# Performance work log

Hardware: AMD Instinct MI355X
Metric: run time of the kernel (lower is better)

## Reference

```python
import jax, jax.numpy as jnp
import numpy as np

N_NODES = 50000
N_EDGES = 640000
DIM_IN = 128
DIM_OUT = 128
NUM_GRAPHS = 64


def setup_inputs() -> dict:
    key = jax.random.key(0)
    ks = jax.random.split(key, 8)
    x = jax.random.normal(ks[0], (N_NODES, DIM_IN), dtype=jnp.float32)
    edge_index = jax.random.randint(ks[1], (2, N_EDGES), 0, N_NODES, dtype=jnp.int32)
    batch = jnp.sort(jax.random.randint(ks[2], (N_NODES,), 0, NUM_GRAPHS, dtype=jnp.int32))
    s = 1.0 / np.sqrt(DIM_IN)
    W1 = jax.random.normal(ks[3], (DIM_IN, DIM_IN), dtype=jnp.float32) * s
    W2 = jax.random.normal(ks[4], (DIM_IN, DIM_IN), dtype=jnp.float32) * s
    Wlin = jax.random.normal(ks[5], (DIM_IN, DIM_OUT), dtype=jnp.float32) * s
    b1 = jnp.zeros((DIM_IN,), jnp.float32)
    b2 = jnp.zeros((DIM_IN,), jnp.float32)
    blin = jnp.zeros((DIM_OUT,), jnp.float32)
    return {"x": x, "edge_index": edge_index, "batch": batch,
            "W1": W1, "b1": b1, "W2": W2, "b2": b2, "Wlin": Wlin, "blin": blin}


def _gcn_conv(x, W, b, src, dst, n_nodes):
    # GCNConv: symmetric norm with self-loops: D^{-1/2}(A+I)D^{-1/2} X W + b
    h = x @ W                                                   # [N, d]
    deg = jax.ops.segment_sum(jnp.ones_like(dst, jnp.float32), dst,
                              num_segments=n_nodes) + 1.0       # +1 self loop
    dinv = jax.lax.rsqrt(deg)                                   # [N]
    w = dinv[src] * dinv[dst]                                   # per-edge norm [E]
    agg = jax.ops.segment_sum(h[src] * w[:, None], dst, num_segments=n_nodes)
    return agg + h * (dinv * dinv)[:, None] + b                 # self-loop term + bias


def reference(x, edge_index, batch, W1, b1, W2, b2, Wlin, blin):
    n = x.shape[0]
    src, dst = edge_index[0], edge_index[1]
    h = jax.nn.relu(_gcn_conv(x, W1, b1, src, dst, n))          # dropout = identity (eval)
    h = _gcn_conv(h, W2, b2, src, dst, n)
    # global mean pool over graphs
    s = jax.ops.segment_sum(h, batch, num_segments=NUM_GRAPHS)  # [G, d]
    cnt = jax.ops.segment_sum(jnp.ones((n,), jnp.float32), batch, num_segments=NUM_GRAPHS)
    pooled = s / jnp.maximum(cnt, 1.0)[:, None]
    return jax.nn.relu(pooled @ Wlin + blin)
```

## Files before the change

### kernel.cpp

```cpp
#include <hip/hip_runtime.h>

#define N_NODES   50000
#define N_EDGES   640000
#define DIM       128
#define NUM_GRAPHS 64
#define SLOTS     64

typedef __attribute__((ext_vector_type(8))) short          s16x8;
typedef __attribute__((ext_vector_type(8))) unsigned short u16x8;
typedef __attribute__((ext_vector_type(4))) float          f32x4;

__device__ inline float bf2f(unsigned short u) {
    unsigned v = ((unsigned)u) << 16;
    float f;
    __builtin_memcpy(&f, &v, 4);
    return f;
}
__device__ inline unsigned short f2bf(float f) {
    unsigned u;
    __builtin_memcpy(&u, &f, 4);
    u = (u + 0x7fffu + ((u >> 16) & 1u)) >> 16;
    return (unsigned short)u;
}

__global__ __launch_bounds__(128) void k_prep_w(const float* __restrict__ W1,
                                                const float* __restrict__ W2,
                                                unsigned short* __restrict__ Wt1,
                                                unsigned short* __restrict__ Wt2,
                                                int* __restrict__ cnt,
                                                float* __restrict__ pooled) {
    int k = blockIdx.x & 127;
    const float*    W  = (blockIdx.x < DIM) ? W1 : W2;
    unsigned short* Wt = (blockIdx.x < DIM) ? Wt1 : Wt2;
    int n = threadIdx.x;
    Wt[n * DIM + k] = f2bf(W[k * DIM + n]);

    int gid = blockIdx.x * 128 + threadIdx.x;
    for (int i = gid; i < N_NODES; i += 32768) cnt[i] = 0;
    if (gid < NUM_GRAPHS * DIM) pooled[gid] = 0.f;
}

__global__ __launch_bounds__(256) void k_fill_slots(const int* __restrict__ src,
                                                    const int* __restrict__ dst,
                                                    int* __restrict__ cnt,
                                                    unsigned short* __restrict__ slots) {
    int e0 = (blockIdx.x * blockDim.x + threadIdx.x) * 4;
    if (e0 >= N_EDGES) return;
    int4 s4 = *reinterpret_cast<const int4*>(src + e0);
    int4 d4 = *reinterpret_cast<const int4*>(dst + e0);
    int p0 = atomicAdd(&cnt[d4.x], 1);
    int p1 = atomicAdd(&cnt[d4.y], 1);
    int p2 = atomicAdd(&cnt[d4.z], 1);
    int p3 = atomicAdd(&cnt[d4.w], 1);
    if (p0 < SLOTS) slots[d4.x * SLOTS + p0] = (unsigned short)s4.x;
    if (p1 < SLOTS) slots[d4.y * SLOTS + p1] = (unsigned short)s4.y;
    if (p2 < SLOTS) slots[d4.z * SLOTS + p2] = (unsigned short)s4.z;
    if (p3 < SLOTS) slots[d4.w * SLOTS + p3] = (unsigned short)s4.w;
}

template<int A_F32>
__global__ __launch_bounds__(512) void k_gemm_mfma(const void* __restrict__ Ain,
                                                   const unsigned short* __restrict__ Wt,
                                                   unsigned short* __restrict__ H,
                                                   int M) {
    __shared__ unsigned short wsh[DIM][136];
    const int tid = threadIdx.x;

    #pragma unroll
    for (int i = 0; i < 4; i++) {
        int off = tid * 8 + i * 4096;
        int r = off >> 7, cc = off & 127;
        u16x8 v = *reinterpret_cast<const u16x8*>(Wt + off);
        *reinterpret_cast<u16x8*>(&wsh[r][cc]) = v;
    }
    __syncthreads();

    const int wid  = tid >> 6;
    const int lane = tid & 63;
    const int l15  = lane & 15;
    const int lk   = lane >> 4;
    const int row0 = blockIdx.x * 256 + wid * 32;

    f32x4 acc[2][8];
    #pragma unroll
    for (int a = 0; a < 2; a++)
        #pragma unroll
        for (int n = 0; n < 8; n++) acc[a][n] = (f32x4){0.f, 0.f, 0.f, 0.f};

    const long long r0 = min(row0 + l15,      M - 1);
    const long long r1 = min(row0 + 16 + l15, M - 1);

    #pragma unroll
    for (int kk = 0; kk < 4; kk++) {
        const int kb = kk * 32 + lk * 8;
        s16x8 a0, a1;
        if (A_F32) {
            const float* Af = (const float*)Ain;
            const float4 p0 = *reinterpret_cast<const float4*>(Af + r0 * DIM + kb);
            const float4 q0 = *reinterpret_cast<const float4*>(Af + r0 * DIM + kb + 4);
            const float4 p1 = *reinterpret_cast<const float4*>(Af + r1 * DIM + kb);
            const float4 q1 = *reinterpret_cast<const float4*>(Af + r1 * DIM + kb + 4);
            a0[0]=(short)f2bf(p0.x); a0[1]=(short)f2bf(p0.y); a0[2]=(short)f2bf(p0.z); a0[3]=(short)f2bf(p0.w);
            a0[4]=(short)f2bf(q0.x); a0[5]=(short)f2bf(q0.y); a0[6]=(short)f2bf(q0.z); a0[7]=(short)f2bf(q0.w);
            a1[0]=(short)f2bf(p1.x); a1[1]=(short)f2bf(p1.y); a1[2]=(short)f2bf(p1.z); a1[3]=(short)f2bf(p1.w);
            a1[4]=(short)f2bf(q1.x); a1[5]=(short)f2bf(q1.y); a1[6]=(short)f2bf(q1.z); a1[7]=(short)f2bf(q1.w);
        } else {
            const unsigned short* Ab = (const unsigned short*)Ain;
            a0 = *reinterpret_cast<const s16x8*>(Ab + r0 * DIM + kb);
            a1 = *reinterpret_cast<const s16x8*>(Ab + r1 * DIM + kb);
        }
        #pragma unroll
        for (int n = 0; n < 8; n++) {
            s16x8 b = *reinterpret_cast<const s16x8*>(&wsh[n * 16 + l15][kb]);
            acc[0][n] = __builtin_amdgcn_mfma_f32_16x16x32_bf16(a0, b, acc[0][n], 0, 0, 0);
            acc[1][n] = __builtin_amdgcn_mfma_f32_16x16x32_bf16(a1, b, acc[1][n], 0, 0, 0);
        }
    }

    #pragma unroll
    for (int rh = 0; rh < 2; rh++) {
        #pragma unroll
        for (int j = 0; j < 4; j++) {
            int row = row0 + rh * 16 + lk * 4 + j;
            if (row < M) {
                #pragma unroll
                for (int n = 0; n < 8; n++)
                    H[(long long)row * DIM + n * 16 + l15] = f2bf(acc[rh][n][j]);
            }
        }
    }
}

__device__ inline void gather_node(const int* __restrict__ cnt,
                                   const unsigned short* __restrict__ slots,
                                   const unsigned short* __restrict__ h,
                                   const float* __restrict__ bias,
                                   int n, int c, float dn, float* acc) {
    float d2 = dn * dn;
    u16x8 hv = *reinterpret_cast<const u16x8*>(h + (size_t)n * DIM + c);
    #pragma unroll
    for (int j = 0; j < 8; j++) acc[j] = bf2f(hv[j]) * d2 + bias[c + j];

    const int m = min(cnt[n], SLOTS);
    const unsigned short* sl = slots + (size_t)n * SLOTS;

    int i = 0;
    for (; i + 3 < m; i += 4) {
        int s0 = sl[i], s1 = sl[i + 1], s2 = sl[i + 2], s3 = sl[i + 3];
        float w0 = rsqrtf((float)cnt[s0] + 1.0f) * dn;
        float w1 = rsqrtf((float)cnt[s1] + 1.0f) * dn;
        float w2 = rsqrtf((float)cnt[s2] + 1.0f) * dn;
        float w3 = rsqrtf((float)cnt[s3] + 1.0f) * dn;
        u16x8 v0 = *reinterpret_cast<const u16x8*>(h + (size_t)s0 * DIM + c);
        u16x8 v1 = *reinterpret_cast<const u16x8*>(h + (size_t)s1 * DIM + c);
        u16x8 v2 = *reinterpret_cast<const u16x8*>(h + (size_t)s2 * DIM + c);
        u16x8 v3 = *reinterpret_cast<const u16x8*>(h + (size_t)s3 * DIM + c);
        #pragma unroll
        for (int j = 0; j < 8; j++)
            acc[j] += (bf2f(v0[j]) * w0 + bf2f(v1[j]) * w1) +
                      (bf2f(v2[j]) * w2 + bf2f(v3[j]) * w3);
    }
    for (; i < m; i++) {
        int s0 = sl[i];
        float w0 = rsqrtf((float)cnt[s0] + 1.0f) * dn;
        u16x8 v0 = *reinterpret_cast<const u16x8*>(h + (size_t)s0 * DIM + c);
        #pragma unroll
        for (int j = 0; j < 8; j++) acc[j] += bf2f(v0[j]) * w0;
    }
}

__global__ __launch_bounds__(256) void k_pull1(const int* __restrict__ cnt,
                                               const unsigned short* __restrict__ slots,
                                               const unsigned short* __restrict__ h,
                                               const float* __restrict__ bias,
                                               unsigned short* __restrict__ outp) {
    int gid = blockIdx.x * blockDim.x + threadIdx.x;
    int n = gid >> 4;
    if (n >= N_NODES) return;
    int c = (gid & 15) << 3;

    float dn = rsqrtf((float)cnt[n] + 1.0f);
    float acc[8];
    gather_node(cnt, slots, h, bias, n, c, dn, acc);

    u16x8 o;
    #pragma unroll
    for (int j = 0; j < 8; j++) o[j] = f2bf(fmaxf(acc[j], 0.f));
    *reinterpret_cast<u16x8*>(outp + (size_t)n * DIM + c) = o;
}

__global__ __launch_bounds__(256) void k_pull_pool(const int* __restrict__ cnt,
                                                   const unsigned short* __restrict__ slots,
                                                   const unsigned short* __restrict__ h,
                                                   const float* __restrict__ bias,
                                                   const int* __restrict__ batch,
                                                   float* __restrict__ pooled) {
    __shared__ float pool_l[2][DIM];
    const int tid  = threadIdx.x;
    const int base = blockIdx.x * 16;
    const int n    = base + (tid >> 4);
    const int c    = (tid & 15) << 3;

    pool_l[tid >> 7][tid & 127] = 0.f;
    __syncthreads();

    float dn = rsqrtf((float)cnt[n] + 1.0f);
    float acc[8];
    gather_node(cnt, slots, h, bias, n, c, dn, acc);

    const int g    = batch[n];
    const int gmin = batch[base];
    const int d    = g - gmin;

    if (__all(g == __shfl(g, 0))) {
        #pragma unroll
        for (int j = 0; j < 8; j++) {
            acc[j] += __shfl_xor(acc[j], 16);
            acc[j] += __shfl_xor(acc[j], 32);
        }
        if ((tid & 63) < 16) {
            if (d < 2) {
                #pragma unroll
                for (int j = 0; j < 8; j++) atomicAdd(&pool_l[d][c + j], acc[j]);
            } else {
                #pragma unroll
                for (int j = 0; j < 8; j++) atomicAdd(&pooled[g * DIM + c + j], acc[j]);
            }
        }
    } else {
        if (d < 2) {
            #pragma unroll
            for (int j = 0; j < 8; j++) atomicAdd(&pool_l[d][c + j], acc[j]);
        } else {
            #pragma unroll
            for (int j = 0; j < 8; j++) atomicAdd(&pooled[g * DIM + c + j], acc[j]);
        }
    }
    __syncthreads();

    const int f = tid & 127;
    if (tid < 128) {
        atomicAdd(&pooled[gmin * DIM + f], pool_l[0][f]);
    } else {
        int gmax = batch[base + 15];
        if (gmax > gmin) atomicAdd(&pooled[(gmin + 1) * DIM + f], pool_l[1][f]);
    }
}

__global__ __launch_bounds__(128) void k_pool2(const float* __restrict__ pooled,
                                               const int* __restrict__ batch,
                                               const float* __restrict__ Wlin,
                                               const float* __restrict__ blin,
                                               float* __restrict__ out) {
    int g = blockIdx.x;
    int t = threadIdx.x;
    __shared__ int se[2];
    __shared__ float pr[DIM];
    if (t < 2) {
        int target = g + t;
        int lo = 0, hi = N_NODES;
        while (lo < hi) { int mid = (lo + hi) >> 1; if (batch[mid] < target) lo = mid + 1; else hi = mid; }
        se[t] = lo;
    }
    __syncthreads();
    float inv_cnt = 1.0f / fmaxf((float)(se[1] - se[0]), 1.0f);
    pr[t] = pooled[g * DIM + t] * inv_cnt;
    __syncthreads();
    float acc = blin[t];
    #pragma unroll 8
    for (int k = 0; k < DIM; k++) acc += pr[k] * Wlin[k * DIM + t];
    out[g * DIM + t] = fmaxf(acc, 0.f);
}

extern "C" void kernel_launch(void* const* d_in, const int* in_sizes, int n_in,
                              void* d_out, int out_size, void* d_ws, size_t ws_size,
                              hipStream_t stream) {
    const float* x          = (const float*)d_in[0];
    const int*   edge_index = (const int*)d_in[1];
    const int*   batch      = (const int*)d_in[2];
    const float* W1         = (const float*)d_in[3];
    const float* b1         = (const float*)d_in[4];
    const float* W2         = (const float*)d_in[5];
    const float* b2         = (const float*)d_in[6];
    const float* Wlin       = (const float*)d_in[7];
    const float* blin       = (const float*)d_in[8];
    float*       out        = (float*)d_out;

    const int* src = edge_index;
    const int* dst = edge_index + N_EDGES;

    char* ws = (char*)d_ws;
    size_t off = 0;
    auto alloc = [&](size_t bytes) { void* p = ws + off; off = (off + bytes + 255) & ~255ULL; return p; };
    int*            cnt    = (int*)            alloc((size_t)N_NODES * 4);
    unsigned short* slots  = (unsigned short*) alloc((size_t)N_NODES * SLOTS * 2);
    float*          pooled = (float*)          alloc((size_t)NUM_GRAPHS * DIM * 4);
    unsigned short* Wt1    = (unsigned short*) alloc((size_t)DIM * DIM * 2);
    unsigned short* Wt2    = (unsigned short*) alloc((size_t)DIM * DIM * 2);
    unsigned short* H1     = (unsigned short*) alloc((size_t)N_NODES * DIM * 2);
    unsigned short* Z1     = (unsigned short*) alloc((size_t)N_NODES * DIM * 2);
    unsigned short* H2     = (unsigned short*) alloc((size_t)N_NODES * DIM * 2);

    const int fillBlocks = (N_EDGES / 4 + 255) / 256;
    const int pullBlocks = (N_NODES * 16 + 255) / 256;
    const int gemmBlocks = (N_NODES + 255) / 256;

    k_prep_w<<<2 * DIM, DIM, 0, stream>>>(W1, W2, Wt1, Wt2, cnt, pooled);

    k_fill_slots<<<fillBlocks, 256, 0, stream>>>(src, dst, cnt, slots);

    k_gemm_mfma<1><<<gemmBlocks, 512, 0, stream>>>(x, Wt1, H1, N_NODES);
    k_pull1<<<pullBlocks, 256, 0, stream>>>(cnt, slots, H1, b1, Z1);

    k_gemm_mfma<0><<<gemmBlocks, 512, 0, stream>>>(Z1, Wt2, H2, N_NODES);
    k_pull_pool<<<pullBlocks, 256, 0, stream>>>(cnt, slots, H2, b2, batch, pooled);

    k_pool2<<<NUM_GRAPHS, 128, 0, stream>>>(pooled, batch, Wlin, blin, out);
}
```

Measured before the change: 127.4 us.

## Fuse edge-slot fill with first GEMM and layer-1 gather with second GEMM

The edge-slot fill and the first node GEMM now run as one launch, with a block-index split: the first blocks do the GEMM and the rest do the atomic slot fill. The layer-1 aggregation is fused with the second GEMM. Each block gathers 32 nodes into LDS and multiplies them by W2 with MFMA, so the Z1 intermediate is never written to or read from global memory. This removes two launches and a full N×128 bf16 round trip through memory. In exchange, the second GEMM reads W2 from global memory per wave rather than from LDS, and it uses small 32-row tiles.

```diff
diff --git a/kernel.cpp b/kernel.cpp
--- a/kernel.cpp
+++ b/kernel.cpp
@@ -5,6 +5,8 @@
 #define DIM       128
 #define NUM_GRAPHS 64
 #define SLOTS     64
+#define GEMM1_BLOCKS 196
+#define FILL_BLOCKS  313
 
 typedef __attribute__((ext_vector_type(8))) short          s16x8;
 typedef __attribute__((ext_vector_type(8))) unsigned short u16x8;
@@ -40,37 +42,37 @@
     if (gid < NUM_GRAPHS * DIM) pooled[gid] = 0.f;
 }
 
-__global__ __launch_bounds__(256) void k_fill_slots(const int* __restrict__ src,
+__global__ __launch_bounds__(512) void k_fill_gemm1(const int* __restrict__ src,
                                                     const int* __restrict__ dst,
                                                     int* __restrict__ cnt,
-                                                    unsigned short* __restrict__ slots) {
-    int e0 = (blockIdx.x * blockDim.x + threadIdx.x) * 4;
-    if (e0 >= N_EDGES) return;
-    int4 s4 = *reinterpret_cast<const int4*>(src + e0);
-    int4 d4 = *reinterpret_cast<const int4*>(dst + e0);
-    int p0 = atomicAdd(&cnt[d4.x], 1);
-    int p1 = atomicAdd(&cnt[d4.y], 1);
-    int p2 = atomicAdd(&cnt[d4.z], 1);
-    int p3 = atomicAdd(&cnt[d4.w], 1);
-    if (p0 < SLOTS) slots[d4.x * SLOTS + p0] = (unsigned short)s4.x;
-    if (p1 < SLOTS) slots[d4.y * SLOTS + p1] = (unsigned short)s4.y;
-    if (p2 < SLOTS) slots[d4.z * SLOTS + p2] = (unsigned short)s4.z;
-    if (p3 < SLOTS) slots[d4.w * SLOTS + p3] = (unsigned short)s4.w;
-}
-
-template<int A_F32>
-__global__ __launch_bounds__(512) void k_gemm_mfma(const void* __restrict__ Ain,
-                                                   const unsigned short* __restrict__ Wt,
-                                                   unsigned short* __restrict__ H,
-                                                   int M) {
+                                                    unsigned short* __restrict__ slots,
+                                                    const float* __restrict__ x,
+                                                    const unsigned short* __restrict__ Wt1,
+                                                    unsigned short* __restrict__ H1) {
     __shared__ unsigned short wsh[DIM][136];
     const int tid = threadIdx.x;
+
+    if (blockIdx.x >= GEMM1_BLOCKS) {
+        int e0 = ((blockIdx.x - GEMM1_BLOCKS) * 512 + tid) * 4;
+        if (e0 >= N_EDGES) return;
+        int4 s4 = *reinterpret_cast<const int4*>(src + e0);
+        int4 d4 = *reinterpret_cast<const int4*>(dst + e0);
+        int p0 = atomicAdd(&cnt[d4.x], 1);
+        int p1 = atomicAdd(&cnt[d4.y], 1);
+        int p2 = atomicAdd(&cnt[d4.z], 1);
+        int p3 = atomicAdd(&cnt[d4.w], 1);
+        if (p0 < SLOTS) slots[d4.x * SLOTS + p0] = (unsigned short)s4.x;
+        if (p1 < SLOTS) slots[d4.y * SLOTS + p1] = (unsigned short)s4.y;
+        if (p2 < SLOTS) slots[d4.z * SLOTS + p2] = (unsigned short)s4.z;
+        if (p3 < SLOTS) slots[d4.w * SLOTS + p3] = (unsigned short)s4.w;
+        return;
+    }
 
     #pragma unroll
     for (int i = 0; i < 4; i++) {
         int off = tid * 8 + i * 4096;
         int r = off >> 7, cc = off & 127;
-        u16x8 v = *reinterpret_cast<const u16x8*>(Wt + off);
+        u16x8 v = *reinterpret_cast<const u16x8*>(Wt1 + off);
         *reinterpret_cast<u16x8*>(&wsh[r][cc]) = v;
     }
     __syncthreads();
@@ -87,28 +89,21 @@
         #pragma unroll
         for (int n = 0; n < 8; n++) acc[a][n] = (f32x4){0.f, 0.f, 0.f, 0.f};
 
-    const long long r0 = min(row0 + l15,      M - 1);
-    const long long r1 = min(row0 + 16 + l15, M - 1);
+    const long long r0 = min(row0 + l15,      N_NODES - 1);
+    const long long r1 = min(row0 + 16 + l15, N_NODES - 1);
 
     #pragma unroll
     for (int kk = 0; kk < 4; kk++) {
         const int kb = kk * 32 + lk * 8;
         s16x8 a0, a1;
-        if (A_F32) {
-            const float* Af = (const float*)Ain;
-            const float4 p0 = *reinterpret_cast<const float4*>(Af + r0 * DIM + kb);
-            const float4 q0 = *reinterpret_cast<const float4*>(Af + r0 * DIM + kb + 4);
-            const float4 p1 = *reinterpret_cast<const float4*>(Af + r1 * DIM + kb);
-            const float4 q1 = *reinterpret_cast<const float4*>(Af + r1 * DIM + kb + 4);
-            a0[0]=(short)f2bf(p0.x); a0[1]=(short)f2bf(p0.y); a0[2]=(short)f2bf(p0.z); a0[3]=(short)f2bf(p0.w);
-            a0[4]=(short)f2bf(q0.x); a0[5]=(short)f2bf(q0.y); a0[6]=(short)f2bf(q0.z); a0[7]=(short)f2bf(q0.w);
-            a1[0]=(short)f2bf(p1.x); a1[1]=(short)f2bf(p1.y); a1[2]=(short)f2bf(p1.z); a1[3]=(short)f2bf(p1.w);
-            a1[4]=(short)f2bf(q1.x); a1[5]=(short)f2bf(q1.y); a1[6]=(short)f2bf(q1.z); a1[7]=(short)f2bf(q1.w);
-        } else {
-            const unsigned short* Ab = (const unsigned short*)Ain;
-            a0 = *reinterpret_cast<const s16x8*>(Ab + r0 * DIM + kb);
-            a1 = *reinterpret_cast<const s16x8*>(Ab + r1 * DIM + kb);
-        }
+        const float4 p0 = *reinterpret_cast<const float4*>(x + r0 * DIM + kb);
+        const float4 q0 = *reinterpret_cast<const float4*>(x + r0 * DIM + kb + 4);
+        const float4 p1 = *reinterpret_cast<const float4*>(x + r1 * DIM + kb);
+        const float4 q1 = *reinterpret_cast<const float4*>(x + r1 * DIM + kb + 4);
+        a0[0]=(short)f2bf(p0.x); a0[1]=(short)f2bf(p0.y); a0[2]=(short)f2bf(p0.z); a0[3]=(short)f2bf(p0.w);
+        a0[4]=(short)f2bf(q0.x); a0[5]=(short)f2bf(q0.y); a0[6]=(short)f2bf(q0.z); a0[7]=(short)f2bf(q0.w);
+        a1[0]=(short)f2bf(p1.x); a1[1]=(short)f2bf(p1.y); a1[2]=(short)f2bf(p1.z); a1[3]=(short)f2bf(p1.w);
+        a1[4]=(short)f2bf(q1.x); a1[5]=(short)f2bf(q1.y); a1[6]=(short)f2bf(q1.z); a1[7]=(short)f2bf(q1.w);
         #pragma unroll
         for (int n = 0; n < 8; n++) {
             s16x8 b = *reinterpret_cast<const s16x8*>(&wsh[n * 16 + l15][kb]);
@@ -122,10 +117,10 @@
         #pragma unroll
         for (int j = 0; j < 4; j++) {
             int row = row0 + rh * 16 + lk * 4 + j;
-            if (row < M) {
+            if (row < N_NODES) {
                 #pragma unroll
                 for (int n = 0; n < 8; n++)
-                    H[(long long)row * DIM + n * 16 + l15] = f2bf(acc[rh][n][j]);
+                    H1[(long long)row * DIM + n * 16 + l15] = f2bf(acc[rh][n][j]);
             }
         }
     }
@@ -169,24 +164,62 @@
     }
 }
 
-__global__ __launch_bounds__(256) void k_pull1(const int* __restrict__ cnt,
-                                               const unsigned short* __restrict__ slots,
-                                               const unsigned short* __restrict__ h,
-                                               const float* __restrict__ bias,
-                                               unsigned short* __restrict__ outp) {
-    int gid = blockIdx.x * blockDim.x + threadIdx.x;
-    int n = gid >> 4;
-    if (n >= N_NODES) return;
-    int c = (gid & 15) << 3;
-
-    float dn = rsqrtf((float)cnt[n] + 1.0f);
-    float acc[8];
-    gather_node(cnt, slots, h, bias, n, c, dn, acc);
-
-    u16x8 o;
-    #pragma unroll
-    for (int j = 0; j < 8; j++) o[j] = f2bf(fmaxf(acc[j], 0.f));
-    *reinterpret_cast<u16x8*>(outp + (size_t)n * DIM + c) = o;
+__global__ __launch_bounds__(512) void k_pull1g(const int* __restrict__ cnt,
+                                                const unsigned short* __restrict__ slots,
+                                                const unsigned short* __restrict__ h,
+                                                const float* __restrict__ bias,
+                                                const unsigned short* __restrict__ Wt2,
+                                                unsigned short* __restrict__ H2) {
+    __shared__ unsigned short zl[32][136];
+    const int tid  = threadIdx.x;
+    const int base = blockIdx.x * 32;
+    const int ln   = tid >> 4;
+    const int n    = base + ln;
+    const int c    = (tid & 15) << 3;
+
+    u16x8 o = (u16x8){0, 0, 0, 0, 0, 0, 0, 0};
+    if (n < N_NODES) {
+        float dn = rsqrtf((float)cnt[n] + 1.0f);
+        float acc[8];
+        gather_node(cnt, slots, h, bias, n, c, dn, acc);
+        #pragma unroll
+        for (int j = 0; j < 8; j++) o[j] = f2bf(fmaxf(acc[j], 0.f));
+    }
+    *reinterpret_cast<u16x8*>(&zl[ln][c]) = o;
+    __syncthreads();
+
+    const int wid = tid >> 6;
+    const int lane = tid & 63;
+    const int l15 = lane & 15;
+    const int lk  = lane >> 4;
+    const int rh  = wid >> 2;
+    const int cp  = (wid & 3) * 2;
+
+    f32x4 accm[2];
+    accm[0] = (f32x4){0.f, 0.f, 0.f, 0.f};
+    accm[1] = (f32x4){0.f, 0.f, 0.f, 0.f};
+
+    #pragma unroll
+    for (int kk = 0; kk < 4; kk++) {
+        const int kb = kk * 32 + lk * 8;
+        s16x8 a = *reinterpret_cast<const s16x8*>(&zl[rh * 16 + l15][kb]);
+        #pragma unroll
+        for (int t2 = 0; t2 < 2; t2++) {
+            s16x8 b = *reinterpret_cast<const s16x8*>(Wt2 + (size_t)((cp + t2) * 16 + l15) * DIM + kb);
+            accm[t2] = __builtin_amdgcn_mfma_f32_16x16x32_bf16(a, b, accm[t2], 0, 0, 0);
+        }
+    }
+
+    #pragma unroll
+    for (int t2 = 0; t2 < 2; t2++) {
+        const int col = (cp + t2) * 16 + l15;
+        #pragma unroll
+        for (int j = 0; j < 4; j++) {
+            int row = base + rh * 16 + lk * 4 + j;
+            if (row < N_NODES)
+                H2[(size_t)row * DIM + col] = f2bf(accm[t2][j]);
+        }
+    }
 }
 
 __global__ __launch_bounds__(256) void k_pull_pool(const int* __restrict__ cnt,
@@ -298,21 +331,17 @@
     unsigned short* Wt1    = (unsigned short*) alloc((size_t)DIM * DIM * 2);
     unsigned short* Wt2    = (unsigned short*) alloc((size_t)DIM * DIM * 2);
     unsigned short* H1     = (unsigned short*) alloc((size_t)N_NODES * DIM * 2);
-    unsigned short* Z1     = (unsigned short*) alloc((size_t)N_NODES * DIM * 2);
     unsigned short* H2     = (unsigned short*) alloc((size_t)N_NODES * DIM * 2);
 
-    const int fillBlocks = (N_EDGES / 4 + 255) / 256;
-    const int pullBlocks = (N_NODES * 16 + 255) / 256;
-    const int gemmBlocks = (N_NODES + 255) / 256;
+    const int pull1Blocks = (N_NODES + 31) / 32;
+    const int pullBlocks  = (N_NODES * 16 + 255) / 256;
 
     k_prep_w<<<2 * DIM, DIM, 0, stream>>>(W1, W2, Wt1, Wt2, cnt, pooled);
 
-    k_fill_slots<<<fillBlocks, 256, 0, stream>>>(src, dst, cnt, slots);
-
-    k_gemm_mfma<1><<<gemmBlocks, 512, 0, stream>>>(x, Wt1, H1, N_NODES);
-    k_pull1<<<pullBlocks, 256, 0, stream>>>(cnt, slots, H1, b1, Z1);
-
-    k_gemm_mfma<0><<<gemmBlocks, 512, 0, stream>>>(Z1, Wt2, H2, N_NODES);
+    k_fill_gemm1<<<GEMM1_BLOCKS + FILL_BLOCKS, 512, 0, stream>>>(src, dst, cnt, slots, x, Wt1, H1);
+
+    k_pull1g<<<pull1Blocks, 512, 0, stream>>>(cnt, slots, H1, b1, Wt2, H2);
+
     k_pull_pool<<<pullBlocks, 256, 0, stream>>>(cnt, slots, H2, b2, batch, pooled);
 
     k_pool2<<<NUM_GRAPHS, 128, 0, stream>>>(pooled, batch, Wlin, blin, out);
```

New measurement: 126.2 us. Within noise of the previous version (-0.9%).
